# Kernel tuning notes

Measured on AMD Instinct MI355X. Metric: run time of the kernel, lower is better.

Reference implementation:

```python
import jax, jax.numpy as jnp
import numpy as np

B, T, N, H, L = 64, 256, 512, 1024, 2


def setup_inputs() -> dict:
    key = jax.random.key(0)
    ks = jax.random.split(key, 12)
    s = 0.02  # weight init scale
    return {
        "x": jax.random.normal(ks[0], (B, T, N), jnp.float32),
        "h": jax.random.normal(ks[1], (L, B, H), jnp.float32),
        "c": jax.random.normal(ks[2], (L, B, H), jnp.float32),
        # layer 0: input dim N
        "W_ih0": jax.random.normal(ks[3], (4 * H, N), jnp.float32) * s,
        "W_hh0": jax.random.normal(ks[4], (4 * H, H), jnp.float32) * s,
        "b_ih0": jax.random.normal(ks[5], (4 * H,), jnp.float32) * s,
        "b_hh0": jax.random.normal(ks[6], (4 * H,), jnp.float32) * s,
        # layer 1: input dim H
        "W_ih1": jax.random.normal(ks[7], (4 * H, H), jnp.float32) * s,
        "W_hh1": jax.random.normal(ks[8], (4 * H, H), jnp.float32) * s,
        "b_ih1": jax.random.normal(ks[9], (4 * H,), jnp.float32) * s,
        "b_hh1": jax.random.normal(ks[10], (4 * H,), jnp.float32) * s,
    }


def _lstm_cell(x_t, h_l, c_l, Wi, Wh, bi, bh):
    # gates: [B, 4H], torch LSTMCell gate order i, f, g, o
    gates = x_t @ Wi.T + h_l @ Wh.T + bi + bh
    i, f, g, o = jnp.split(gates, 4, axis=-1)
    i, f, o = jax.nn.sigmoid(i), jax.nn.sigmoid(f), jax.nn.sigmoid(o)
    g = jnp.tanh(g)
    c_new = f * c_l + i * g
    h_new = o * jnp.tanh(c_new)
    return h_new, c_new


def reference(x, h, c, W_ih0, W_hh0, b_ih0, b_hh0, W_ih1, W_hh1, b_ih1, b_hh1):
    params = [(W_ih0, W_hh0, b_ih0, b_hh0), (W_ih1, W_hh1, b_ih1, b_hh1)]

    def step(carry, x_t):
        h, c = carry  # each [L, B, H]
        inp = x_t
        new_h, new_c = [], []
        for l, (Wi, Wh, bi, bh) in enumerate(params):
            h_new, c_new = _lstm_cell(inp, h[l], c[l], Wi, Wh, bi, bh)
            new_h.append(h_new)
            new_c.append(c_new)
            inp = h_new
        return (jnp.stack(new_h), jnp.stack(new_c)), inp

    xT = jnp.swapaxes(x, 0, 1)  # [T, B, N]
    (h_final, c_final), outsT = jax.lax.scan(step, (h, c), xT)
    outs = jnp.swapaxes(outsT, 0, 1)  # [B, T, H]
    return outs, h_final, c_final
```

## Files before the change

### kernel.cpp

```cpp
#include <hip/hip_runtime.h>
#include <hip/hip_bf16.h>


#define T_ 256
#define B_ 64
#define N_ 512
#define H_ 1024
#define FH_ 4096
#define NWG_SEQ 256
#define BH_ (B_ * H_)

typedef _Float16 f16;
typedef _Float16 f16x4 __attribute__((ext_vector_type(4)));
typedef _Float16 f16x8 __attribute__((ext_vector_type(8)));
typedef float f32x4 __attribute__((ext_vector_type(4)));

template <bool V> struct BC { static constexpr bool value = V; };

__device__ __forceinline__ float sigf(float x) { return 1.f / (1.f + __expf(-x)); }
__device__ __forceinline__ float tanhf_fast(float x) { return 1.f - 2.f / (__expf(2.f * x) + 1.f); }

__device__ __forceinline__ void st_u64g(unsigned long long* p, unsigned long long v) {
  __hip_atomic_store(p, v, __ATOMIC_RELAXED, __HIP_MEMORY_SCOPE_AGENT);
}
__device__ __forceinline__ f16x8 ld_b128_nc(const f16* p) {
  f16x8 r;
  asm volatile("global_load_dwordx4 %0, %1, off sc0 sc1" : "=v"(r) : "v"(p));
  return r;
}

__global__ __launch_bounds__(256) void init_all(
    const float* __restrict__ x, const float* __restrict__ h,
    const float* __restrict__ Wih0, const float* __restrict__ bih0, const float* __restrict__ bhh0,
    const float* __restrict__ Whh0, const float* __restrict__ Wih1, const float* __restrict__ Whh1,
    const float* __restrict__ bih1, const float* __restrict__ bhh1,
    f16* __restrict__ xT, f16* __restrict__ wih0, f16* __restrict__ whh0,
    f16* __restrict__ wih1, f16* __restrict__ whh1,
    float* __restrict__ bias0, float* __restrict__ bias1,
    f16* __restrict__ hinit, unsigned* __restrict__ cnt)
{
  const int stride = gridDim.x * blockDim.x;
  const int t0 = blockIdx.x * blockDim.x + threadIdx.x;

  for (int i = t0; i < T_ * B_ * N_; i += stride) {
    int n = i & (N_ - 1);
    int tb = i >> 9;
    int b = tb & (B_ - 1);
    int t = tb >> 6;
    xT[i] = (f16)x[((size_t)b * T_ + t) * N_ + n];
  }
  for (int i = t0; i < FH_ * N_; i += stride) wih0[i] = (f16)Wih0[i];
  for (int i = t0; i < FH_ * H_; i += stride) {
    whh0[i] = (f16)Whh0[i];
    wih1[i] = (f16)Wih1[i];
    whh1[i] = (f16)Whh1[i];
  }
  for (int i = t0; i < FH_; i += stride) {
    bias0[i] = bih0[i] + bhh0[i];
    bias1[i] = bih1[i] + bhh1[i];
  }
  for (int i = t0; i < 2 * BH_; i += stride) hinit[i] = (f16)h[i];
  if (t0 < 1024) cnt[t0] = 0u;
}

__global__ __launch_bounds__(256) void gemm_pre0(
    const f16* __restrict__ xT, const f16* __restrict__ wih0,
    const float* __restrict__ bias0, f16* __restrict__ pre0T)
{
  const int wid = threadIdx.x >> 6;
  const int lane = threadIdx.x & 63;
  const int lr = lane & 15;
  const int lkq = (lane >> 4) << 3;
  const int lrq = (lane >> 4) << 2;

  const int mt = blockIdx.x & 255;
  const int ct = (blockIdx.x >> 8) * 4 + wid;
  const int row0 = mt * 64, col0 = ct * 64;

  f32x4 acc[4][4] = {};
  const f16* Abase = xT + (size_t)row0 * N_;

  #pragma unroll 2
  for (int kk = 0; kk < N_ / 32; ++kk) {
    const int k = kk * 32 + lkq;
    f16x8 a[4], b[4];
    #pragma unroll
    for (int r = 0; r < 4; ++r)
      a[r] = *(const f16x8*)(Abase + (size_t)(r * 16 + lr) * N_ + k);
    #pragma unroll
    for (int cf = 0; cf < 4; ++cf)
      b[cf] = *(const f16x8*)(wih0 + (size_t)(col0 + cf * 16 + lr) * N_ + k);
    #pragma unroll
    for (int r = 0; r < 4; ++r)
      #pragma unroll
      for (int cf = 0; cf < 4; ++cf)
        acc[r][cf] = __builtin_amdgcn_mfma_f32_16x16x32_f16(a[r], b[cf], acc[r][cf], 0, 0, 0);
  }

  #pragma unroll
  for (int r = 0; r < 4; ++r) {
    #pragma unroll
    for (int cf = 0; cf < 4; ++cf) {
      const int col = col0 + cf * 16 + lr;
      const float bv = bias0[col];
      f16x4 pv;
      #pragma unroll
      for (int ri = 0; ri < 4; ++ri) pv[ri] = (f16)(acc[r][cf][ri] + bv);
      *(f16x4*)(pre0T + ((size_t)mt * FH_ + col) * 64 + r * 16 + lrq) = pv;
    }
  }
}

__global__ __launch_bounds__(256, 1) void lstm_seq(
    const f16* __restrict__ pre0T, const f16* __restrict__ whh0,
    const f16* __restrict__ wih1, const f16* __restrict__ whh1,
    const float* __restrict__ bias1, const f16* __restrict__ hinit,
    const float* __restrict__ cin,
    f16* __restrict__ h0buf, f16* __restrict__ h1buf,
    float* __restrict__ out, unsigned* __restrict__ cnt)
{
  __shared__ __align__(16) float exc[2][4][32][33];
  __shared__ __align__(16) f16 smH[2][32][8];

  const int tid = threadIdx.x;
  const int p = tid >> 6;
  const int lane = tid & 63;
  const int lr = lane & 15;
  const int lq = lane >> 4;
  const int lkq = lq << 3;
  const int lrq = lq << 2;

  const int wg = blockIdx.x;
  const int pod = wg >> 7;
  const int slot = wg & 127;
  const int rs = pod << 5;
  const int ub = slot << 3;
  unsigned* podcnt = cnt + (pod << 9);

  f16x8 l0w[2][8], l1aw[2][8], l1bw[2][8];
  #pragma unroll
  for (int cf = 0; cf < 2; ++cf) {
    const size_t wr = (size_t)((2 * cf + (lr >> 3)) * H_ + ub + (lr & 7)) * H_;
    #pragma unroll
    for (int j = 0; j < 8; ++j) {
      const int k = (p * 8 + j) * 32 + lkq;
      l0w[cf][j]  = *(const f16x8*)(whh0 + wr + k);
      l1aw[cf][j] = *(const f16x8*)(wih1 + wr + k);
      l1bw[cf][j] = *(const f16x8*)(whh1 + wr + k);
    }
  }

  const int crow = tid & 31;
  const int cu = tid >> 5;
  const size_t cell = (size_t)(rs + crow) * H_ + ub + cu;
  float c0 = cin[cell];
  float c1 = cin[(size_t)BH_ + cell];
  float b1v[4];
  #pragma unroll
  for (int g = 0; g < 4; ++g) b1v[g] = bias1[g * H_ + ub + cu];

  float* outh = out + (size_t)B_ * T_ * H_;
  float* outc = outh + 2 * BH_;

  auto body = [&](auto A0c, auto A1c, int e) {
    constexpr bool A0 = decltype(A0c)::value;
    constexpr bool A1 = decltype(A1c)::value;

    float pf[4];
    if (A0) {
      #pragma unroll
      for (int g = 0; g < 4; ++g)
        pf[g] = (float)pre0T[((size_t)e * FH_ + g * H_ + ub + cu) * 64 + rs + crow];
    }

    if (e > 0) {
      if (tid == 0) {
        while (__hip_atomic_load(&podcnt[e - 1], __ATOMIC_RELAXED, __HIP_MEMORY_SCOPE_AGENT) < 128u)
          __builtin_amdgcn_s_sleep(2);
      }
      __syncthreads();
    }

    const f16* h0s = ((e == 0) ? hinit : h0buf + (size_t)((e - 1) & 1) * BH_) + (size_t)rs * H_;
    const f16* h1s = A1 ? (((e == 1) ? hinit + BH_ : h1buf + (size_t)(e & 1) * BH_) + (size_t)rs * H_)
                        : (const f16*)nullptr;
    f16x8 a0v[8], a1v[8], c0v[8], c1v[8];
    #pragma unroll
    for (int j = 0; j < 8; ++j) {
      const int k = (p * 8 + j) * 32 + lkq;
      a0v[j] = ld_b128_nc(h0s + (size_t)lr * H_ + k);
      a1v[j] = ld_b128_nc(h0s + (size_t)(16 + lr) * H_ + k);
    }
    if (A1) {
      #pragma unroll
      for (int j = 0; j < 8; ++j) {
        const int k = (p * 8 + j) * 32 + lkq;
        c0v[j] = ld_b128_nc(h1s + (size_t)lr * H_ + k);
        c1v[j] = ld_b128_nc(h1s + (size_t)(16 + lr) * H_ + k);
      }
    }
    asm volatile("s_waitcnt vmcnt(0)" ::: "memory");
    __builtin_amdgcn_sched_barrier(0);

    f32x4 acc0[2][2] = {};
    f32x4 acc1[2][2] = {};
    #pragma unroll
    for (int j = 0; j < 8; ++j) {
      if (A0) {
        #pragma unroll
        for (int cf = 0; cf < 2; ++cf) {
          acc0[cf][0] = __builtin_amdgcn_mfma_f32_16x16x32_f16(a0v[j], l0w[cf][j], acc0[cf][0], 0, 0, 0);
          acc0[cf][1] = __builtin_amdgcn_mfma_f32_16x16x32_f16(a1v[j], l0w[cf][j], acc0[cf][1], 0, 0, 0);
        }
      }
      if (A1) {
        #pragma unroll
        for (int cf = 0; cf < 2; ++cf) {
          acc1[cf][0] = __builtin_amdgcn_mfma_f32_16x16x32_f16(a0v[j], l1aw[cf][j], acc1[cf][0], 0, 0, 0);
          acc1[cf][1] = __builtin_amdgcn_mfma_f32_16x16x32_f16(a1v[j], l1aw[cf][j], acc1[cf][1], 0, 0, 0);
        }
      }
    }
    if (A1) {
      #pragma unroll
      for (int j = 0; j < 8; ++j) {
        #pragma unroll
        for (int cf = 0; cf < 2; ++cf) {
          acc1[cf][0] = __builtin_amdgcn_mfma_f32_16x16x32_f16(c0v[j], l1bw[cf][j], acc1[cf][0], 0, 0, 0);
          acc1[cf][1] = __builtin_amdgcn_mfma_f32_16x16x32_f16(c1v[j], l1bw[cf][j], acc1[cf][1], 0, 0, 0);
        }
      }
    }

    #pragma unroll
    for (int cf = 0; cf < 2; ++cf)
      #pragma unroll
      for (int rf = 0; rf < 2; ++rf)
        #pragma unroll
        for (int ri = 0; ri < 4; ++ri) {
          if (A0) exc[0][p][rf * 16 + lrq + ri][cf * 16 + lr] = acc0[cf][rf][ri];
          if (A1) exc[1][p][rf * 16 + lrq + ri][cf * 16 + lr] = acc1[cf][rf][ri];
        }
    __syncthreads();

    if (A0) {
      float gv[4];
      #pragma unroll
      for (int g = 0; g < 4; ++g)
        gv[g] = exc[0][0][crow][g * 8 + cu] + exc[0][1][crow][g * 8 + cu]
              + exc[0][2][crow][g * 8 + cu] + exc[0][3][crow][g * 8 + cu] + pf[g];
      const float cn = sigf(gv[1]) * c0 + sigf(gv[0]) * tanhf_fast(gv[2]);
      const float hn = sigf(gv[3]) * tanhf_fast(cn);
      c0 = cn;
      smH[0][crow][cu] = (f16)hn;
      if (e == T_ - 1) { outh[cell] = hn; outc[cell] = cn; }
    }
    if (A1) {
      const int t = e - 1;
      float gv[4];
      #pragma unroll
      for (int g = 0; g < 4; ++g)
        gv[g] = exc[1][0][crow][g * 8 + cu] + exc[1][1][crow][g * 8 + cu]
              + exc[1][2][crow][g * 8 + cu] + exc[1][3][crow][g * 8 + cu] + b1v[g];
      const float cn = sigf(gv[1]) * c1 + sigf(gv[0]) * tanhf_fast(gv[2]);
      const float hn = sigf(gv[3]) * tanhf_fast(cn);
      c1 = cn;
      smH[1][crow][cu] = (f16)hn;
      out[(size_t)(rs + crow) * (T_ * H_) + (size_t)t * H_ + ub + cu] = hn;
      if (e == T_) { outh[BH_ + cell] = hn; outc[BH_ + cell] = cn; }
    }
    __syncthreads();

    if (A0 && p == 0) {
      const int row = lane >> 1, half = lane & 1;
      unsigned long long v = *(const unsigned long long*)&smH[0][row][half * 4];
      st_u64g((unsigned long long*)(h0buf + (size_t)(e & 1) * BH_
                                    + (size_t)(rs + row) * H_ + ub + half * 4), v);
    }
    if (A1 && p == 1) {
      const int row = lane >> 1, half = lane & 1;
      unsigned long long v = *(const unsigned long long*)&smH[1][row][half * 4];
      st_u64g((unsigned long long*)(h1buf + (size_t)((e - 1) & 1) * BH_
                                    + (size_t)(rs + row) * H_ + ub + half * 4), v);
    }
    asm volatile("s_waitcnt vmcnt(0)" ::: "memory");
    __syncthreads();
    if (tid == 0)
      (void)__hip_atomic_fetch_add(&podcnt[e], 1u, __ATOMIC_RELAXED, __HIP_MEMORY_SCOPE_AGENT);
  };

  body(BC<true>{}, BC<false>{}, 0);
  for (int e = 1; e < T_; ++e) body(BC<true>{}, BC<true>{}, e);
  body(BC<false>{}, BC<true>{}, T_);
}

extern "C" void kernel_launch(void* const* d_in, const int* in_sizes, int n_in,
                              void* d_out, int out_size, void* d_ws, size_t ws_size,
                              hipStream_t stream)
{
  const float* x    = (const float*)d_in[0];
  const float* h    = (const float*)d_in[1];
  const float* c    = (const float*)d_in[2];
  const float* Wih0 = (const float*)d_in[3];
  const float* Whh0 = (const float*)d_in[4];
  const float* bih0 = (const float*)d_in[5];
  const float* bhh0 = (const float*)d_in[6];
  const float* Wih1 = (const float*)d_in[7];
  const float* Whh1 = (const float*)d_in[8];
  const float* bih1 = (const float*)d_in[9];
  const float* bhh1 = (const float*)d_in[10];

  char* w = (char*)d_ws;
  size_t off = 0;
  auto carve = [&](size_t bytes) -> char* {
    char* ptr = w + off;
    off = (off + bytes + 255) & ~(size_t)255;
    return ptr;
  };
  f16*   pre0T = (f16*)  carve((size_t)T_ * B_ * FH_ * 2);
  f16*   xT    = (f16*)  carve((size_t)T_ * B_ * N_ * 2);
  f16*   wih0  = (f16*)  carve((size_t)FH_ * N_ * 2);
  f16*   whh0  = (f16*)  carve((size_t)FH_ * H_ * 2);
  f16*   wih1  = (f16*)  carve((size_t)FH_ * H_ * 2);
  f16*   whh1  = (f16*)  carve((size_t)FH_ * H_ * 2);
  float* bias0 = (float*)carve((size_t)FH_ * 4);
  float* bias1 = (float*)carve((size_t)FH_ * 4);
  f16*   hinit = (f16*)  carve((size_t)2 * BH_ * 2);
  f16*   h0buf = (f16*)  carve((size_t)2 * BH_ * 2);
  f16*   h1buf = (f16*)  carve((size_t)2 * BH_ * 2);
  unsigned* cnt = (unsigned*)carve(1024 * 4);
  if (off > ws_size) return;

  init_all<<<2048, 256, 0, stream>>>(x, h, Wih0, bih0, bhh0, Whh0, Wih1, Whh1, bih1, bhh1,
                                     xT, wih0, whh0, wih1, whh1, bias0, bias1, hinit, cnt);
  gemm_pre0<<<4096, 256, 0, stream>>>(xT, wih0, bias0, pre0T);
  lstm_seq<<<NWG_SEQ, 256, 0, stream>>>(pre0T, whh0, wih1, whh1, bias1, hinit, (const float*)c,
                                        h0buf, h1buf, (float*)d_out, cnt);
}
```

Before: 2.362 ms.

## Split layer barriers into per-layer counters and use full-depth hidden-state rings

```diff
diff --git a/kernel.cpp b/kernel.cpp
--- a/kernel.cpp
+++ b/kernel.cpp
@@ -60,7 +60,7 @@
     bias1[i] = bih1[i] + bhh1[i];
   }
   for (int i = t0; i < 2 * BH_; i += stride) hinit[i] = (f16)h[i];
-  if (t0 < 1024) cnt[t0] = 0u;
+  if (t0 < 2048) cnt[t0] = 0u;
 }
 
 __global__ __launch_bounds__(256) void gemm_pre0(
@@ -111,11 +111,13 @@
   }
 }
 
+template <bool DEEP>
 __global__ __launch_bounds__(256, 1) void lstm_seq(
     const f16* __restrict__ pre0T, const f16* __restrict__ whh0,
     const f16* __restrict__ wih1, const f16* __restrict__ whh1,
     const float* __restrict__ bias1, const f16* __restrict__ hinit,
     const float* __restrict__ cin,
+    f16* __restrict__ h0ring, f16* __restrict__ h1ring,
     f16* __restrict__ h0buf, f16* __restrict__ h1buf,
     float* __restrict__ out, unsigned* __restrict__ cnt)
 {
@@ -135,7 +137,8 @@
   const int slot = wg & 127;
   const int rs = pod << 5;
   const int ub = slot << 3;
-  unsigned* podcnt = cnt + (pod << 9);
+  unsigned* podc0 = cnt + (size_t)(pod * 2) * 512;
+  unsigned* podc1 = cnt + (size_t)(pod * 2 + 1) * 512;
 
   f16x8 l0w[2][8], l1aw[2][8], l1bw[2][8];
   #pragma unroll
@@ -162,6 +165,14 @@
   float* outh = out + (size_t)B_ * T_ * H_;
   float* outc = outh + 2 * BH_;
 
+  auto poll = [&](unsigned* word) {
+    if (tid == 0) {
+      while (__hip_atomic_load(word, __ATOMIC_RELAXED, __HIP_MEMORY_SCOPE_AGENT) < 128u)
+        __builtin_amdgcn_s_sleep(1);
+    }
+    __syncthreads();
+  };
+
   auto body = [&](auto A0c, auto A1c, int e) {
     constexpr bool A0 = decltype(A0c)::value;
     constexpr bool A1 = decltype(A1c)::value;
@@ -173,34 +184,27 @@
         pf[g] = (float)pre0T[((size_t)e * FH_ + g * H_ + ub + cu) * 64 + rs + crow];
     }
 
-    if (e > 0) {
-      if (tid == 0) {
-        while (__hip_atomic_load(&podcnt[e - 1], __ATOMIC_RELAXED, __HIP_MEMORY_SCOPE_AGENT) < 128u)
-          __builtin_amdgcn_s_sleep(2);
-      }
-      __syncthreads();
-    }
-
-    const f16* h0s = ((e == 0) ? hinit : h0buf + (size_t)((e - 1) & 1) * BH_) + (size_t)rs * H_;
-    const f16* h1s = A1 ? (((e == 1) ? hinit + BH_ : h1buf + (size_t)(e & 1) * BH_) + (size_t)rs * H_)
-                        : (const f16*)nullptr;
-    f16x8 a0v[8], a1v[8], c0v[8], c1v[8];
+    if (e > 0) poll(&podc0[e - 1]);
+
+    const f16* h0s = ((e == 0) ? hinit
+                      : (DEEP ? h0ring + (size_t)(e - 1) * BH_
+                              : h0buf + (size_t)((e - 1) & 1) * BH_)) + (size_t)rs * H_;
+    f16x8 a0v[8], a1v[8];
     #pragma unroll
     for (int j = 0; j < 8; ++j) {
       const int k = (p * 8 + j) * 32 + lkq;
-      a0v[j] = ld_b128_nc(h0s + (size_t)lr * H_ + k);
-      a1v[j] = ld_b128_nc(h0s + (size_t)(16 + lr) * H_ + k);
-    }
-    if (A1) {
-      #pragma unroll
-      for (int j = 0; j < 8; ++j) {
-        const int k = (p * 8 + j) * 32 + lkq;
-        c0v[j] = ld_b128_nc(h1s + (size_t)lr * H_ + k);
-        c1v[j] = ld_b128_nc(h1s + (size_t)(16 + lr) * H_ + k);
-      }
-    }
-    asm volatile("s_waitcnt vmcnt(0)" ::: "memory");
-    __builtin_amdgcn_sched_barrier(0);
+      if (DEEP) {
+        a0v[j] = *(const f16x8*)(h0s + (size_t)lr * H_ + k);
+        a1v[j] = *(const f16x8*)(h0s + (size_t)(16 + lr) * H_ + k);
+      } else {
+        a0v[j] = ld_b128_nc(h0s + (size_t)lr * H_ + k);
+        a1v[j] = ld_b128_nc(h0s + (size_t)(16 + lr) * H_ + k);
+      }
+    }
+    if (!DEEP) {
+      asm volatile("s_waitcnt vmcnt(0)" ::: "memory");
+      __builtin_amdgcn_sched_barrier(0);
+    }
 
     f32x4 acc0[2][2] = {};
     f32x4 acc1[2][2] = {};
@@ -221,29 +225,17 @@
         }
       }
     }
-    if (A1) {
-      #pragma unroll
-      for (int j = 0; j < 8; ++j) {
-        #pragma unroll
-        for (int cf = 0; cf < 2; ++cf) {
-          acc1[cf][0] = __builtin_amdgcn_mfma_f32_16x16x32_f16(c0v[j], l1bw[cf][j], acc1[cf][0], 0, 0, 0);
-          acc1[cf][1] = __builtin_amdgcn_mfma_f32_16x16x32_f16(c1v[j], l1bw[cf][j], acc1[cf][1], 0, 0, 0);
-        }
-      }
-    }
-
-    #pragma unroll
-    for (int cf = 0; cf < 2; ++cf)
-      #pragma unroll
-      for (int rf = 0; rf < 2; ++rf)
-        #pragma unroll
-        for (int ri = 0; ri < 4; ++ri) {
-          if (A0) exc[0][p][rf * 16 + lrq + ri][cf * 16 + lr] = acc0[cf][rf][ri];
-          if (A1) exc[1][p][rf * 16 + lrq + ri][cf * 16 + lr] = acc1[cf][rf][ri];
-        }
-    __syncthreads();
 
     if (A0) {
+      #pragma unroll
+      for (int cf = 0; cf < 2; ++cf)
+        #pragma unroll
+        for (int rf = 0; rf < 2; ++rf)
+          #pragma unroll
+          for (int ri = 0; ri < 4; ++ri)
+            exc[0][p][rf * 16 + lrq + ri][cf * 16 + lr] = acc0[cf][rf][ri];
+      __syncthreads();
+
       float gv[4];
       #pragma unroll
       for (int g = 0; g < 4; ++g)
@@ -254,8 +246,60 @@
       c0 = cn;
       smH[0][crow][cu] = (f16)hn;
       if (e == T_ - 1) { outh[cell] = hn; outc[cell] = cn; }
-    }
+      __syncthreads();
+
+      if (p == 0) {
+        const int row = lane >> 1, half = lane & 1;
+        unsigned long long v = *(const unsigned long long*)&smH[0][row][half * 4];
+        f16* dst = DEEP ? h0ring + (size_t)e * BH_ : h0buf + (size_t)(e & 1) * BH_;
+        st_u64g((unsigned long long*)(dst + (size_t)(rs + row) * H_ + ub + half * 4), v);
+      }
+      asm volatile("s_waitcnt vmcnt(0)" ::: "memory");
+      if (tid == 0)
+        (void)__hip_atomic_fetch_add(&podc0[e], 1u, __ATOMIC_RELAXED, __HIP_MEMORY_SCOPE_AGENT);
+    }
+
     if (A1) {
+      if (e >= 2) poll(&podc1[e - 1]);
+
+      const f16* h1s = ((e == 1) ? hinit + BH_
+                        : (DEEP ? h1ring + (size_t)(e - 2) * BH_
+                                : h1buf + (size_t)(e & 1) * BH_)) + (size_t)rs * H_;
+      f16x8 c0v[8], c1v[8];
+      #pragma unroll
+      for (int j = 0; j < 8; ++j) {
+        const int k = (p * 8 + j) * 32 + lkq;
+        if (DEEP) {
+          c0v[j] = *(const f16x8*)(h1s + (size_t)lr * H_ + k);
+          c1v[j] = *(const f16x8*)(h1s + (size_t)(16 + lr) * H_ + k);
+        } else {
+          c0v[j] = ld_b128_nc(h1s + (size_t)lr * H_ + k);
+          c1v[j] = ld_b128_nc(h1s + (size_t)(16 + lr) * H_ + k);
+        }
+      }
+      if (!DEEP) {
+        asm volatile("s_waitcnt vmcnt(0)" ::: "memory");
+        __builtin_amdgcn_sched_barrier(0);
+      }
+
+      #pragma unroll
+      for (int j = 0; j < 8; ++j) {
+        #pragma unroll
+        for (int cf = 0; cf < 2; ++cf) {
+          acc1[cf][0] = __builtin_amdgcn_mfma_f32_16x16x32_f16(c0v[j], l1bw[cf][j], acc1[cf][0], 0, 0, 0);
+          acc1[cf][1] = __builtin_amdgcn_mfma_f32_16x16x32_f16(c1v[j], l1bw[cf][j], acc1[cf][1], 0, 0, 0);
+        }
+      }
+
+      #pragma unroll
+      for (int cf = 0; cf < 2; ++cf)
+        #pragma unroll
+        for (int rf = 0; rf < 2; ++rf)
+          #pragma unroll
+          for (int ri = 0; ri < 4; ++ri)
+            exc[1][p][rf * 16 + lrq + ri][cf * 16 + lr] = acc1[cf][rf][ri];
+      __syncthreads();
+
       const int t = e - 1;
       float gv[4];
       #pragma unroll
@@ -268,25 +312,18 @@
       smH[1][crow][cu] = (f16)hn;
       out[(size_t)(rs + crow) * (T_ * H_) + (size_t)t * H_ + ub + cu] = hn;
       if (e == T_) { outh[BH_ + cell] = hn; outc[BH_ + cell] = cn; }
-    }
-    __syncthreads();
-
-    if (A0 && p == 0) {
-      const int row = lane >> 1, half = lane & 1;
-      unsigned long long v = *(const unsigned long long*)&smH[0][row][half * 4];
-      st_u64g((unsigned long long*)(h0buf + (size_t)(e & 1) * BH_
-                                    + (size_t)(rs + row) * H_ + ub + half * 4), v);
-    }
-    if (A1 && p == 1) {
-      const int row = lane >> 1, half = lane & 1;
-      unsigned long long v = *(const unsigned long long*)&smH[1][row][half * 4];
-      st_u64g((unsigned long long*)(h1buf + (size_t)((e - 1) & 1) * BH_
-                                    + (size_t)(rs + row) * H_ + ub + half * 4), v);
-    }
-    asm volatile("s_waitcnt vmcnt(0)" ::: "memory");
-    __syncthreads();
-    if (tid == 0)
-      (void)__hip_atomic_fetch_add(&podcnt[e], 1u, __ATOMIC_RELAXED, __HIP_MEMORY_SCOPE_AGENT);
+      __syncthreads();
+
+      if (p == 1) {
+        const int row = lane >> 1, half = lane & 1;
+        unsigned long long v = *(const unsigned long long*)&smH[1][row][half * 4];
+        f16* dst = DEEP ? h1ring + (size_t)(e - 1) * BH_ : h1buf + (size_t)((e - 1) & 1) * BH_;
+        st_u64g((unsigned long long*)(dst + (size_t)(rs + row) * H_ + ub + half * 4), v);
+      }
+      asm volatile("s_waitcnt vmcnt(0)" ::: "memory");
+      if (tid == 64)
+        (void)__hip_atomic_fetch_add(&podc1[e], 1u, __ATOMIC_RELAXED, __HIP_MEMORY_SCOPE_AGENT);
+    }
   };
 
   body(BC<true>{}, BC<false>{}, 0);
@@ -328,12 +365,22 @@
   f16*   hinit = (f16*)  carve((size_t)2 * BH_ * 2);
   f16*   h0buf = (f16*)  carve((size_t)2 * BH_ * 2);
   f16*   h1buf = (f16*)  carve((size_t)2 * BH_ * 2);
-  unsigned* cnt = (unsigned*)carve(1024 * 4);
-  if (off > ws_size) return;
+  unsigned* cnt = (unsigned*)carve(2048 * 4);
+  const size_t base_end = off;
+  f16*   h0ring = (f16*) carve((size_t)T_ * BH_ * 2);
+  f16*   h1ring = (f16*) carve((size_t)T_ * BH_ * 2);
+  const bool deep = (off <= ws_size);
+  if (base_end > ws_size) return;
 
   init_all<<<2048, 256, 0, stream>>>(x, h, Wih0, bih0, bhh0, Whh0, Wih1, Whh1, bih1, bhh1,
                                      xT, wih0, whh0, wih1, whh1, bias0, bias1, hinit, cnt);
   gemm_pre0<<<4096, 256, 0, stream>>>(xT, wih0, bias0, pre0T);
-  lstm_seq<<<NWG_SEQ, 256, 0, stream>>>(pre0T, whh0, wih1, whh1, bias1, hinit, (const float*)c,
-                                        h0buf, h1buf, (float*)d_out, cnt);
-}
+  if (deep)
+    lstm_seq<true><<<NWG_SEQ, 256, 0, stream>>>(pre0T, whh0, wih1, whh1, bias1, hinit,
+                                                (const float*)c, h0ring, h1ring, h0buf, h1buf,
+                                                (float*)d_out, cnt);
+  else
+    lstm_seq<false><<<NWG_SEQ, 256, 0, stream>>>(pre0T, whh0, wih1, whh1, bias1, hinit,
+                                                 (const float*)c, h0ring, h1ring, h0buf, h1buf,
+                                                 (float*)d_out, cnt);
+}
```

Result: faster. 1.934 ms (-18.1%).

## Replace atomic counters with per-slot flags and per-timestep hidden-state ring

Applied to the files above, without the earlier changes.

```diff
diff --git a/kernel.cpp b/kernel.cpp
--- a/kernel.cpp
+++ b/kernel.cpp
@@ -14,19 +14,31 @@
 typedef _Float16 f16x4 __attribute__((ext_vector_type(4)));
 typedef _Float16 f16x8 __attribute__((ext_vector_type(8)));
 typedef float f32x4 __attribute__((ext_vector_type(4)));
+typedef unsigned long long ull;
 
 template <bool V> struct BC { static constexpr bool value = V; };
 
 __device__ __forceinline__ float sigf(float x) { return 1.f / (1.f + __expf(-x)); }
 __device__ __forceinline__ float tanhf_fast(float x) { return 1.f - 2.f / (__expf(2.f * x) + 1.f); }
 
-__device__ __forceinline__ void st_u64g(unsigned long long* p, unsigned long long v) {
+__device__ __forceinline__ void st_u64g(ull* p, ull v) {
   __hip_atomic_store(p, v, __ATOMIC_RELAXED, __HIP_MEMORY_SCOPE_AGENT);
+}
+__device__ __forceinline__ void st_u32g(unsigned* p, unsigned v) {
+  __hip_atomic_store(p, v, __ATOMIC_RELAXED, __HIP_MEMORY_SCOPE_AGENT);
+}
+__device__ __forceinline__ ull ld_u64g(const ull* p) {
+  return __hip_atomic_load(p, __ATOMIC_RELAXED, __HIP_MEMORY_SCOPE_AGENT);
 }
 __device__ __forceinline__ f16x8 ld_b128_nc(const f16* p) {
   f16x8 r;
   asm volatile("global_load_dwordx4 %0, %1, off sc0 sc1" : "=v"(r) : "v"(p));
   return r;
+}
+template <bool CACHED>
+__device__ __forceinline__ f16x8 ldf(const f16* p) {
+  if constexpr (CACHED) return *(const f16x8*)p;
+  else return ld_b128_nc(p);
 }
 
 __global__ __launch_bounds__(256) void init_all(
@@ -37,7 +49,7 @@
     f16* __restrict__ xT, f16* __restrict__ wih0, f16* __restrict__ whh0,
     f16* __restrict__ wih1, f16* __restrict__ whh1,
     float* __restrict__ bias0, float* __restrict__ bias1,
-    f16* __restrict__ hinit, unsigned* __restrict__ cnt)
+    f16* __restrict__ hinit, unsigned* __restrict__ flags)
 {
   const int stride = gridDim.x * blockDim.x;
   const int t0 = blockIdx.x * blockDim.x + threadIdx.x;
@@ -60,7 +72,7 @@
     bias1[i] = bih1[i] + bhh1[i];
   }
   for (int i = t0; i < 2 * BH_; i += stride) hinit[i] = (f16)h[i];
-  if (t0 < 1024) cnt[t0] = 0u;
+  if (t0 < 256) flags[t0] = 0u;
 }
 
 __global__ __launch_bounds__(256) void gemm_pre0(
@@ -111,13 +123,14 @@
   }
 }
 
+template <bool DEEP>
 __global__ __launch_bounds__(256, 1) void lstm_seq(
     const f16* __restrict__ pre0T, const f16* __restrict__ whh0,
     const f16* __restrict__ wih1, const f16* __restrict__ whh1,
     const float* __restrict__ bias1, const f16* __restrict__ hinit,
     const float* __restrict__ cin,
-    f16* __restrict__ h0buf, f16* __restrict__ h1buf,
-    float* __restrict__ out, unsigned* __restrict__ cnt)
+    f16* __restrict__ h0r, f16* __restrict__ h1r,
+    float* __restrict__ out, unsigned* __restrict__ flags)
 {
   __shared__ __align__(16) float exc[2][4][32][33];
   __shared__ __align__(16) f16 smH[2][32][8];
@@ -135,7 +148,9 @@
   const int slot = wg & 127;
   const int rs = pod << 5;
   const int ub = slot << 3;
-  unsigned* podcnt = cnt + (pod << 9);
+  unsigned* podflags = flags + (pod << 7);
+
+  auto rt = [&](int t) -> size_t { return DEEP ? (size_t)t : (size_t)(t & 7); };
 
   f16x8 l0w[2][8], l1aw[2][8], l1bw[2][8];
   #pragma unroll
@@ -173,34 +188,39 @@
         pf[g] = (float)pre0T[((size_t)e * FH_ + g * H_ + ub + cu) * 64 + rs + crow];
     }
 
-    if (e > 0) {
-      if (tid == 0) {
-        while (__hip_atomic_load(&podcnt[e - 1], __ATOMIC_RELAXED, __HIP_MEMORY_SCOPE_AGENT) < 128u)
-          __builtin_amdgcn_s_sleep(2);
-      }
-      __syncthreads();
-    }
-
-    const f16* h0s = ((e == 0) ? hinit : h0buf + (size_t)((e - 1) & 1) * BH_) + (size_t)rs * H_;
-    const f16* h1s = A1 ? (((e == 1) ? hinit + BH_ : h1buf + (size_t)(e & 1) * BH_) + (size_t)rs * H_)
+    if (e > 0 && p == 0) {
+      const ull* fp = (const ull*)podflags;
+      for (;;) {
+        ull v = ld_u64g(&fp[lane]);
+        const bool ok = ((unsigned)v >= (unsigned)e) && ((unsigned)(v >> 32) >= (unsigned)e);
+        if (__ballot(ok) == ~0ull) break;
+        __builtin_amdgcn_s_sleep(1);
+      }
+    }
+    __syncthreads();
+
+    const f16* h0s = ((e == 0) ? hinit : h0r + rt(e - 1) * BH_) + (size_t)rs * H_;
+    const f16* h1s = A1 ? (((e == 1) ? hinit + BH_ : h1r + rt(e - 2) * BH_) + (size_t)rs * H_)
                         : (const f16*)nullptr;
     f16x8 a0v[8], a1v[8], c0v[8], c1v[8];
     #pragma unroll
     for (int j = 0; j < 8; ++j) {
       const int k = (p * 8 + j) * 32 + lkq;
-      a0v[j] = ld_b128_nc(h0s + (size_t)lr * H_ + k);
-      a1v[j] = ld_b128_nc(h0s + (size_t)(16 + lr) * H_ + k);
+      a0v[j] = ldf<DEEP>(h0s + (size_t)lr * H_ + k);
+      a1v[j] = ldf<DEEP>(h0s + (size_t)(16 + lr) * H_ + k);
     }
     if (A1) {
       #pragma unroll
       for (int j = 0; j < 8; ++j) {
         const int k = (p * 8 + j) * 32 + lkq;
-        c0v[j] = ld_b128_nc(h1s + (size_t)lr * H_ + k);
-        c1v[j] = ld_b128_nc(h1s + (size_t)(16 + lr) * H_ + k);
-      }
-    }
-    asm volatile("s_waitcnt vmcnt(0)" ::: "memory");
-    __builtin_amdgcn_sched_barrier(0);
+        c0v[j] = ldf<DEEP>(h1s + (size_t)lr * H_ + k);
+        c1v[j] = ldf<DEEP>(h1s + (size_t)(16 + lr) * H_ + k);
+      }
+    }
+    if (!DEEP) {
+      asm volatile("s_waitcnt vmcnt(0)" ::: "memory");
+      __builtin_amdgcn_sched_barrier(0);
+    }
 
     f32x4 acc0[2][2] = {};
     f32x4 acc1[2][2] = {};
@@ -243,50 +263,50 @@
         }
     __syncthreads();
 
+    float hn0 = 0.f, cn0 = 0.f, hn1 = 0.f, cn1 = 0.f;
     if (A0) {
       float gv[4];
       #pragma unroll
       for (int g = 0; g < 4; ++g)
         gv[g] = exc[0][0][crow][g * 8 + cu] + exc[0][1][crow][g * 8 + cu]
               + exc[0][2][crow][g * 8 + cu] + exc[0][3][crow][g * 8 + cu] + pf[g];
-      const float cn = sigf(gv[1]) * c0 + sigf(gv[0]) * tanhf_fast(gv[2]);
-      const float hn = sigf(gv[3]) * tanhf_fast(cn);
-      c0 = cn;
-      smH[0][crow][cu] = (f16)hn;
-      if (e == T_ - 1) { outh[cell] = hn; outc[cell] = cn; }
+      cn0 = sigf(gv[1]) * c0 + sigf(gv[0]) * tanhf_fast(gv[2]);
+      hn0 = sigf(gv[3]) * tanhf_fast(cn0);
+      c0 = cn0;
+      smH[0][crow][cu] = (f16)hn0;
     }
     if (A1) {
-      const int t = e - 1;
       float gv[4];
       #pragma unroll
       for (int g = 0; g < 4; ++g)
         gv[g] = exc[1][0][crow][g * 8 + cu] + exc[1][1][crow][g * 8 + cu]
               + exc[1][2][crow][g * 8 + cu] + exc[1][3][crow][g * 8 + cu] + b1v[g];
-      const float cn = sigf(gv[1]) * c1 + sigf(gv[0]) * tanhf_fast(gv[2]);
-      const float hn = sigf(gv[3]) * tanhf_fast(cn);
-      c1 = cn;
-      smH[1][crow][cu] = (f16)hn;
-      out[(size_t)(rs + crow) * (T_ * H_) + (size_t)t * H_ + ub + cu] = hn;
-      if (e == T_) { outh[BH_ + cell] = hn; outc[BH_ + cell] = cn; }
+      cn1 = sigf(gv[1]) * c1 + sigf(gv[0]) * tanhf_fast(gv[2]);
+      hn1 = sigf(gv[3]) * tanhf_fast(cn1);
+      c1 = cn1;
+      smH[1][crow][cu] = (f16)hn1;
     }
     __syncthreads();
 
     if (A0 && p == 0) {
       const int row = lane >> 1, half = lane & 1;
-      unsigned long long v = *(const unsigned long long*)&smH[0][row][half * 4];
-      st_u64g((unsigned long long*)(h0buf + (size_t)(e & 1) * BH_
-                                    + (size_t)(rs + row) * H_ + ub + half * 4), v);
+      ull v = *(const ull*)&smH[0][row][half * 4];
+      st_u64g((ull*)(h0r + rt(e) * BH_ + (size_t)(rs + row) * H_ + ub + half * 4), v);
     }
     if (A1 && p == 1) {
       const int row = lane >> 1, half = lane & 1;
-      unsigned long long v = *(const unsigned long long*)&smH[1][row][half * 4];
-      st_u64g((unsigned long long*)(h1buf + (size_t)((e - 1) & 1) * BH_
-                                    + (size_t)(rs + row) * H_ + ub + half * 4), v);
+      ull v = *(const ull*)&smH[1][row][half * 4];
+      st_u64g((ull*)(h1r + rt(e - 1) * BH_ + (size_t)(rs + row) * H_ + ub + half * 4), v);
     }
     asm volatile("s_waitcnt vmcnt(0)" ::: "memory");
     __syncthreads();
-    if (tid == 0)
-      (void)__hip_atomic_fetch_add(&podcnt[e], 1u, __ATOMIC_RELAXED, __HIP_MEMORY_SCOPE_AGENT);
+    if (tid == 0) st_u32g(&podflags[slot], (unsigned)(e + 1));
+
+    if (A0 && e == T_ - 1) { outh[cell] = hn0; outc[cell] = cn0; }
+    if (A1) {
+      out[(size_t)(rs + crow) * (T_ * H_) + (size_t)(e - 1) * H_ + ub + cu] = hn1;
+      if (e == T_) { outh[BH_ + cell] = hn1; outc[BH_ + cell] = cn1; }
+    }
   };
 
   body(BC<true>{}, BC<false>{}, 0);
@@ -326,14 +346,24 @@
   float* bias0 = (float*)carve((size_t)FH_ * 4);
   float* bias1 = (float*)carve((size_t)FH_ * 4);
   f16*   hinit = (f16*)  carve((size_t)2 * BH_ * 2);
-  f16*   h0buf = (f16*)  carve((size_t)2 * BH_ * 2);
-  f16*   h1buf = (f16*)  carve((size_t)2 * BH_ * 2);
-  unsigned* cnt = (unsigned*)carve(1024 * 4);
-  if (off > ws_size) return;
+  f16*   h0s   = (f16*)  carve((size_t)8 * BH_ * 2);
+  f16*   h1s   = (f16*)  carve((size_t)8 * BH_ * 2);
+  unsigned* flags = (unsigned*)carve(256 * 4);
+  const size_t base_end = off;
+  f16*   h0ring = (f16*) carve((size_t)T_ * BH_ * 2);
+  f16*   h1ring = (f16*) carve((size_t)T_ * BH_ * 2);
+  const bool deep = (off <= ws_size);
+  if (base_end > ws_size) return;
 
   init_all<<<2048, 256, 0, stream>>>(x, h, Wih0, bih0, bhh0, Whh0, Wih1, Whh1, bih1, bhh1,
-                                     xT, wih0, whh0, wih1, whh1, bias0, bias1, hinit, cnt);
+                                     xT, wih0, whh0, wih1, whh1, bias0, bias1, hinit, flags);
   gemm_pre0<<<4096, 256, 0, stream>>>(xT, wih0, bias0, pre0T);
-  lstm_seq<<<NWG_SEQ, 256, 0, stream>>>(pre0T, whh0, wih1, whh1, bias1, hinit, (const float*)c,
-                                        h0buf, h1buf, (float*)d_out, cnt);
-}
+  if (deep)
+    lstm_seq<true><<<NWG_SEQ, 256, 0, stream>>>(pre0T, whh0, wih1, whh1, bias1, hinit,
+                                                (const float*)c, h0ring, h1ring,
+                                                (float*)d_out, flags);
+  else
+    lstm_seq<false><<<NWG_SEQ, 256, 0, stream>>>(pre0T, whh0, wih1, whh1, bias1, hinit,
+                                                 (const float*)c, h0s, h1s,
+                                                 (float*)d_out, flags);
+}
```

Result: faster. 2.063 ms (-12.6%).
